# Kernel optimization log

Measured on AMD Instinct MI355X. Metric: run time of the kernel, lower is better.

Reference implementation:

```python
import jax, jax.numpy as jnp
import numpy as np

GRID = (32, 32, 32)  # must match init grid_size


def setup_inputs() -> dict:
    key = jax.random.key(0)
    # Mimic the module's init: D = 0.01 everywhere + 0.1 on the 6x6 diagonal,
    # plus small uniform noise so the baseline exercises non-degenerate values.
    D = jax.random.uniform(key, (6, 6, *GRID), dtype=jnp.float32) * 0.02 + 0.01
    D = D.at[jnp.arange(6), jnp.arange(6)].add(0.1)
    return {"D": D, "sx": 1, "sy": 1, "sz": 1, "ex": 30, "ey": 30, "ez": 30,
            "max_iterations": 300}


def reference(D, sx, sy, sz, ex, ey, ez, max_iterations):
    """flash_wave (training path, inference=False): 300-step CA as one lax.scan.

    Returns the stacked history of phi (pre-update, as the torch loop appends
    phi at the top of each iteration): shape [max_iterations, 6, X, Y, Z].
    Early exit is emulated by freezing phi once the wave reaches (ex,ey,ez),
    so no per-step host sync is needed.
    """
    phi0 = jnp.zeros((6, *GRID), dtype=D.dtype).at[:, sx, sy, sz].set(1.0)
    active_D = D + 0.95  # inference=False branch

    def body(carry, _):
        phi, done = carry
        # 6x6 channel mixing per grid cell: 'oixyz,ixyz->oxyz'
        phi_out = jnp.einsum('oixyz,ixyz->oxyz', active_D, phi)
        pn = jnp.zeros_like(phi)
        pn = pn.at[0, 1:, :, :].set(phi_out[0, :-1, :, :])   # +x
        pn = pn.at[1, :-1, :, :].set(phi_out[1, 1:, :, :])   # -x
        pn = pn.at[2, :, 1:, :].set(phi_out[2, :, :-1, :])   # +y
        pn = pn.at[3, :, :-1, :].set(phi_out[3, :, 1:, :])   # -y
        pn = pn.at[4, :, :, 1:].set(phi_out[4, :, :, :-1])   # +z
        pn = pn.at[5, :, :, :-1].set(phi_out[5, :, :, 1:])   # -z
        nxt = jnp.clip(pn, 0.0, 1.0)
        nxt = jnp.where(done, phi, nxt)  # freeze after target reached
        reached = jnp.sum(nxt[:, ex, ey, ez]) > 0.01
        return (nxt, jnp.logical_or(done, reached)), phi

    (_, _), history = jax.lax.scan(body, (phi0, jnp.array(False)), None,
                                   length=int(max_iterations))
    return history
```

## Files before the change

### kernel.cpp

```cpp
#include <hip/hip_runtime.h>

#define NCH 6
#define NX 32
#define PLANE 1024
#define NCELL (NX * PLANE)
#define STEP_STRIDE (NCH * NCELL)
#define NTHREADS 256
#define NBLOCKS 128
#define RB 2

#define RING32_WORDS ((size_t)RB * 4 * NCELL)
#define F_DONE 0

typedef unsigned long long u64;
typedef unsigned int u32;
typedef float fx4 __attribute__((ext_vector_type(4)));

__device__ __forceinline__ u32 ld32(const u32* p) {
    return __hip_atomic_load(p, __ATOMIC_RELAXED, __HIP_MEMORY_SCOPE_AGENT);
}
__device__ __forceinline__ void st32(u32* p, u32 v) {
    __hip_atomic_store(p, v, __ATOMIC_RELAXED, __HIP_MEMORY_SCOPE_AGENT);
}
__device__ __forceinline__ int ldi(const int* p) {
    return __hip_atomic_load(p, __ATOMIC_RELAXED, __HIP_MEMORY_SCOPE_AGENT);
}
__device__ __forceinline__ void sti(int* p, int v) {
    __hip_atomic_store(p, v, __ATOMIC_RELAXED, __HIP_MEMORY_SCOPE_AGENT);
}
__device__ __forceinline__ u32 tagf(float a, unsigned P) {
    const u32 w = __float_as_uint(a);
    return P ? (w | 0x80000000u) : w;
}
__device__ __forceinline__ float untagf(u32 w) {
    return __uint_as_float(w & 0x7fffffffu);
}

__global__ void __launch_bounds__(NTHREADS)
BEMNA_V7_2_PhaseSpace_44117904064519_kernel(
    const float* __restrict__ D,
    const int* __restrict__ sx_p, const int* __restrict__ sy_p,
    const int* __restrict__ sz_p, const int* __restrict__ ex_p,
    const int* __restrict__ ey_p, const int* __restrict__ ez_p,
    const int* __restrict__ maxit_p,
    float* __restrict__ out,
    u32* __restrict__ ring,
    int* __restrict__ flags)
{
    __shared__ float tile[2][2][NTHREADS];
    __shared__ int lds_dn;

    const int tid = (int)threadIdx.x;
    const int bx  = (int)blockIdx.x;
    const int x   = bx >> 2;
    const int s   = bx & 3;
    const int yl  = tid >> 5;
    const int z   = tid & 31;
    const int y   = (s << 3) + yl;
    const int cell = (x << 10) + (y << 5) + z;

    const int sx = *sx_p, sy = *sy_p, sz = *sz_p;
    const int ex = *ex_p, ey = *ey_p, ez = *ez_p;
    const int maxit = *maxit_p;
    const bool is_seed   = (cell == ((sx << 10) | (sy << 5) | sz));
    const bool is_target = (cell == ((ex << 10) | (ey << 5) | ez));

    float dreg[NCH][NCH];
#pragma unroll
    for (int o = 0; o < NCH; ++o)
#pragma unroll
        for (int i = 0; i < NCH; ++i)
            dreg[o][i] = D[(size_t)(o * NCH + i) * NCELL + cell] + 0.95f;

    const bool has_xm  = (x >= 1), has_xp = (x <= 30);
    const bool edge_ym = (yl == 0), edge_yp = (yl == 7);
    const bool has_ym  = edge_ym && (y >= 1);
    const bool has_yp  = edge_yp && (y <= 30);
    const bool pub_d2  = edge_yp && (y <= 30);
    const bool pub_d3  = edge_ym && (y >= 1);

    const float iv = is_seed ? 1.0f : 0.0f;
    float pz4, pz5;
    {
        float po[NCH];
#pragma unroll
        for (int o = 0; o < NCH; ++o) {
            float a = 0.f;
#pragma unroll
            for (int i = 0; i < NCH; ++i) a = fmaf(dreg[o][i], iv, a);
            po[o] = a;
        }
        st32(ring + 0 * NCELL + cell, tagf(po[0], 0));
        st32(ring + 1 * NCELL + cell, tagf(po[1], 0));
        if (pub_d2) st32(ring + 2 * NCELL + cell, tagf(po[2], 0));
        if (pub_d3) st32(ring + 3 * NCELL + cell, tagf(po[3], 0));
        tile[0][0][tid] = po[2];
        tile[0][1][tid] = po[3];
        pz4 = po[4]; pz5 = po[5];
        float* outp = out + cell;
#pragma unroll
        for (int o = 0; o < NCH; ++o)
            __builtin_nontemporal_store(iv, outp + o * NCELL);
    }
    __syncthreads();

    int tripped = 0;
    for (int t = 0; t <= maxit - 2; ++t) {
        const u32* r = ring + (size_t)(t & 1) * 4 * NCELL;
        const unsigned P = (unsigned)((t >> 1) & 1);

        u32 wxm = 0, wxp = 0, wym = 0, wyp = 0;
        int dn = -1, spins = 0;
        for (;;) {
            if (has_xm) wxm = ld32(r + 0 * NCELL + cell - PLANE);
            if (has_xp) wxp = ld32(r + 1 * NCELL + cell + PLANE);
            if (has_ym) wym = ld32(r + 2 * NCELL + cell - 32);
            if (has_yp) wyp = ld32(r + 3 * NCELL + cell + 32);
            dn = ldi(&flags[F_DONE]);
            bool okr = true;
            if (has_xm) okr = okr & ((wxm >> 31) == P);
            if (has_xp) okr = okr & ((wxp >> 31) == P);
            if (has_ym) okr = okr & ((wym >> 31) == P);
            if (has_yp) okr = okr & ((wyp >> 31) == P);
            if (dn >= 0 && t + 1 > dn) break;
            if (__ballot(okr) == ~0ull) break;
            if (spins++) __builtin_amdgcn_s_sleep(1);
        }
        if (tid == 0) lds_dn = dn;
        __syncthreads();
        if (lds_dn >= 0 && t + 1 > lds_dn) break;

        float v[NCH];
        v[0] = has_xm ? untagf(wxm) : 0.0f;
        v[1] = has_xp ? untagf(wxp) : 0.0f;
        v[2] = edge_ym ? (has_ym ? untagf(wym) : 0.0f) : tile[t & 1][0][tid - 32];
        v[3] = edge_yp ? (has_yp ? untagf(wyp) : 0.0f) : tile[t & 1][1][tid + 32];
        const float s4 = __shfl_up(pz4, 1, 32);
        const float s5 = __shfl_down(pz5, 1, 32);
        v[4] = (z >= 1)  ? s4 : 0.0f;
        v[5] = (z <= 30) ? s5 : 0.0f;
#pragma unroll
        for (int o = 0; o < NCH; ++o) v[o] = fminf(fmaxf(v[o], 0.0f), 1.0f);

        if (is_target && !tripped) {
            if (v[0] + v[1] + v[2] + v[3] + v[4] + v[5] > 0.01f) {
                sti(&flags[F_DONE], t + 1);
                tripped = 1;
            }
        }

        float n0 = 0.f, n1 = 0.f, n2 = 0.f, n3 = 0.f, n4 = 0.f, n5 = 0.f;
#pragma unroll
        for (int i = 0; i < NCH; ++i) {
            n0 = fmaf(dreg[0][i], v[i], n0);
            n1 = fmaf(dreg[1][i], v[i], n1);
            n2 = fmaf(dreg[2][i], v[i], n2);
            n3 = fmaf(dreg[3][i], v[i], n3);
            n4 = fmaf(dreg[4][i], v[i], n4);
            n5 = fmaf(dreg[5][i], v[i], n5);
        }

        {
            const unsigned P1 = (unsigned)(((t + 1) >> 1) & 1);
            u32* w = ring + (size_t)((t + 1) & 1) * 4 * NCELL;
            st32(w + 0 * NCELL + cell, tagf(n0, P1));
            st32(w + 1 * NCELL + cell, tagf(n1, P1));
            if (pub_d2) st32(w + 2 * NCELL + cell, tagf(n2, P1));
            if (pub_d3) st32(w + 3 * NCELL + cell, tagf(n3, P1));
            tile[(t + 1) & 1][0][tid] = n2;
            tile[(t + 1) & 1][1][tid] = n3;
            pz4 = n4; pz5 = n5;
        }

        {
            float* outp = out + (size_t)(t + 1) * STEP_STRIDE + cell;
#pragma unroll
            for (int o = 0; o < NCH; ++o)
                __builtin_nontemporal_store(v[o], outp + o * NCELL);
        }
    }
}

__global__ void fill_kernel(const int* __restrict__ flags,
                            float* __restrict__ outf,
                            int total4)
{
    const int s4 = STEP_STRIDE / 4;
    const int maxit = total4 / s4;
    const int ds = flags[F_DONE];
    const int tf = (ds >= 1 && ds <= maxit - 1) ? ds : maxit - 1;
    const int idx = (int)blockIdx.x * (int)blockDim.x + (int)threadIdx.x;
    fx4* o4 = (fx4*)outf;
    const fx4 v = o4[(size_t)tf * s4 + idx];
    for (int t = tf + 1; t < maxit; ++t)
        __builtin_nontemporal_store(v, &o4[(size_t)t * s4 + idx]);
}

extern "C" void kernel_launch(void* const* d_in, const int* in_sizes, int n_in,
                              void* d_out, int out_size, void* d_ws, size_t ws_size,
                              hipStream_t stream)
{
    const float* D   = (const float*)d_in[0];
    const int* sx    = (const int*)d_in[1];
    const int* sy    = (const int*)d_in[2];
    const int* sz    = (const int*)d_in[3];
    const int* ex    = (const int*)d_in[4];
    const int* ey    = (const int*)d_in[5];
    const int* ez    = (const int*)d_in[6];
    const int* maxit = (const int*)d_in[7];
    float* out = (float*)d_out;

    u32* ring  = (u32*)d_ws;
    int* flags = (int*)(ring + RING32_WORDS);

    BEMNA_V7_2_PhaseSpace_44117904064519_kernel<<<dim3(NBLOCKS), dim3(NTHREADS), 0, stream>>>(
        D, sx, sy, sz, ex, ey, ez, maxit, out, ring, flags);

    const int total4 = out_size / 4;
    fill_kernel<<<dim3((STEP_STRIDE / 4) / 256), dim3(256), 0, stream>>>(
        flags, out, total4);
}
```

Measured before the change: 348.1 us.

## Move y-neighbor exchange to wave shuffles and double-buffer spin polling loads

Half of the in-block y-neighbor values now travel between the two rows held by each 64-lane wave through a cross-half shuffle instead of LDS, so only the other half is still read from the shared tile. The cross-block spin-wait is software-pipelined: the next set of ring and flag loads is issued before the previous set is checked, which hides part of the polling latency. The block barrier is replaced by a hand-written LDS waitcnt plus s_barrier with a scheduling fence. This adds branch divergence between odd and even rows and relies on a subtle pairing of odd/even rows per wave and on the correctness of the custom barrier.

```diff
diff --git a/kernel.cpp b/kernel.cpp
--- a/kernel.cpp
+++ b/kernel.cpp
@@ -34,6 +34,14 @@
 }
 __device__ __forceinline__ float untagf(u32 w) {
     return __uint_as_float(w & 0x7fffffffu);
+}
+__device__ __forceinline__ float clip01(float a) {
+    return fminf(fmaxf(a, 0.0f), 1.0f);
+}
+__device__ __forceinline__ void barrier_lds() {
+    asm volatile("s_waitcnt lgkmcnt(0)" ::: "memory");
+    __builtin_amdgcn_s_barrier();
+    __builtin_amdgcn_sched_barrier(0);
 }
 
 __global__ void __launch_bounds__(NTHREADS)
@@ -78,9 +86,10 @@
     const bool has_yp  = edge_yp && (y <= 30);
     const bool pub_d2  = edge_yp && (y <= 30);
     const bool pub_d3  = edge_ym && (y >= 1);
+    const bool odd     = (yl & 1) != 0;
 
     const float iv = is_seed ? 1.0f : 0.0f;
-    float pz4, pz5;
+    float pn2, pn3, pz4, pz5;
     {
         float po[NCH];
 #pragma unroll
@@ -96,7 +105,7 @@
         if (pub_d3) st32(ring + 3 * NCELL + cell, tagf(po[3], 0));
         tile[0][0][tid] = po[2];
         tile[0][1][tid] = po[3];
-        pz4 = po[4]; pz5 = po[5];
+        pn2 = po[2]; pn3 = po[3]; pz4 = po[4]; pz5 = po[5];
         float* outp = out + cell;
 #pragma unroll
         for (int o = 0; o < NCH; ++o)
@@ -109,55 +118,89 @@
         const u32* r = ring + (size_t)(t & 1) * 4 * NCELL;
         const unsigned P = (unsigned)((t >> 1) & 1);
 
-        u32 wxm = 0, wxp = 0, wym = 0, wyp = 0;
-        int dn = -1, spins = 0;
-        for (;;) {
-            if (has_xm) wxm = ld32(r + 0 * NCELL + cell - PLANE);
-            if (has_xp) wxp = ld32(r + 1 * NCELL + cell + PLANE);
-            if (has_ym) wym = ld32(r + 2 * NCELL + cell - 32);
-            if (has_yp) wyp = ld32(r + 3 * NCELL + cell + 32);
-            dn = ldi(&flags[F_DONE]);
-            bool okr = true;
-            if (has_xm) okr = okr & ((wxm >> 31) == P);
-            if (has_xp) okr = okr & ((wxp >> 31) == P);
-            if (has_ym) okr = okr & ((wym >> 31) == P);
-            if (has_yp) okr = okr & ((wyp >> 31) == P);
-            if (dn >= 0 && t + 1 > dn) break;
-            if (__ballot(okr) == ~0ull) break;
-            if (spins++) __builtin_amdgcn_s_sleep(1);
+        const float rz4 = __shfl_up(pz4, 1, 32);
+        const float rz5 = __shfl_down(pz5, 1, 32);
+        const float v4 = (z >= 1)  ? clip01(rz4) : 0.0f;
+        const float v5 = (z <= 30) ? clip01(rz5) : 0.0f;
+        const float sendw = odd ? pn3 : pn2;
+        const float recvw = __shfl_xor(sendw, 32, 64);
+        float v2 = 0.0f, v3 = 0.0f;
+        if (odd) v2 = clip01(recvw); else v3 = clip01(recvw);
+
+        u32 wxm = 0, wxp = 0, wym = 0, wyp = 0; int dn = -1;
+        {
+            const u32* q0 = r + 0 * NCELL + cell - PLANE;
+            const u32* q1 = r + 1 * NCELL + cell + PLANE;
+            const u32* q2 = r + 2 * NCELL + cell - 32;
+            const u32* q3 = r + 3 * NCELL + cell + 32;
+            u32 axm = 0, axp = 0, aym = 0, ayp = 0;
+            u32 bxm = 0, bxp = 0, bym = 0, byp = 0;
+            int adn, bdn;
+            if (has_xm) axm = ld32(q0);
+            if (has_xp) axp = ld32(q1);
+            if (has_ym) aym = ld32(q2);
+            if (has_yp) ayp = ld32(q3);
+            adn = ldi(&flags[F_DONE]);
+            for (;;) {
+                if (has_xm) bxm = ld32(q0);
+                if (has_xp) bxp = ld32(q1);
+                if (has_ym) bym = ld32(q2);
+                if (has_yp) byp = ld32(q3);
+                bdn = ldi(&flags[F_DONE]);
+                bool okr = true;
+                if (has_xm) okr = okr & ((axm >> 31) == P);
+                if (has_xp) okr = okr & ((axp >> 31) == P);
+                if (has_ym) okr = okr & ((aym >> 31) == P);
+                if (has_yp) okr = okr & ((ayp >> 31) == P);
+                if ((adn >= 0 && t + 1 > adn) || __ballot(okr) == ~0ull) {
+                    wxm = axm; wxp = axp; wym = aym; wyp = ayp; dn = adn; break;
+                }
+                if (has_xm) axm = ld32(q0);
+                if (has_xp) axp = ld32(q1);
+                if (has_ym) aym = ld32(q2);
+                if (has_yp) ayp = ld32(q3);
+                adn = ldi(&flags[F_DONE]);
+                okr = true;
+                if (has_xm) okr = okr & ((bxm >> 31) == P);
+                if (has_xp) okr = okr & ((bxp >> 31) == P);
+                if (has_ym) okr = okr & ((bym >> 31) == P);
+                if (has_yp) okr = okr & ((byp >> 31) == P);
+                if ((bdn >= 0 && t + 1 > bdn) || __ballot(okr) == ~0ull) {
+                    wxm = bxm; wxp = bxp; wym = bym; wyp = byp; dn = bdn; break;
+                }
+            }
         }
         if (tid == 0) lds_dn = dn;
-        __syncthreads();
+        barrier_lds();
         if (lds_dn >= 0 && t + 1 > lds_dn) break;
 
-        float v[NCH];
-        v[0] = has_xm ? untagf(wxm) : 0.0f;
-        v[1] = has_xp ? untagf(wxp) : 0.0f;
-        v[2] = edge_ym ? (has_ym ? untagf(wym) : 0.0f) : tile[t & 1][0][tid - 32];
-        v[3] = edge_yp ? (has_yp ? untagf(wyp) : 0.0f) : tile[t & 1][1][tid + 32];
-        const float s4 = __shfl_up(pz4, 1, 32);
-        const float s5 = __shfl_down(pz5, 1, 32);
-        v[4] = (z >= 1)  ? s4 : 0.0f;
-        v[5] = (z <= 30) ? s5 : 0.0f;
-#pragma unroll
-        for (int o = 0; o < NCH; ++o) v[o] = fminf(fmaxf(v[o], 0.0f), 1.0f);
+        const float v0 = has_xm ? clip01(untagf(wxm)) : 0.0f;
+        const float v1 = has_xp ? clip01(untagf(wxp)) : 0.0f;
+        if (odd) {
+            v3 = (yl <= 5) ? clip01(tile[t & 1][1][tid + 32])
+                           : (has_yp ? clip01(untagf(wyp)) : 0.0f);
+        } else {
+            v2 = (yl >= 2) ? clip01(tile[t & 1][0][tid - 32])
+                           : (has_ym ? clip01(untagf(wym)) : 0.0f);
+        }
 
         if (is_target && !tripped) {
-            if (v[0] + v[1] + v[2] + v[3] + v[4] + v[5] > 0.01f) {
+            if (v0 + v1 + v2 + v3 + v4 + v5 > 0.01f) {
                 sti(&flags[F_DONE], t + 1);
                 tripped = 1;
             }
         }
 
+        const float vv[NCH] = { v0, v1, v2, v3, v4, v5 };
         float n0 = 0.f, n1 = 0.f, n2 = 0.f, n3 = 0.f, n4 = 0.f, n5 = 0.f;
 #pragma unroll
         for (int i = 0; i < NCH; ++i) {
-            n0 = fmaf(dreg[0][i], v[i], n0);
-            n1 = fmaf(dreg[1][i], v[i], n1);
-            n2 = fmaf(dreg[2][i], v[i], n2);
-            n3 = fmaf(dreg[3][i], v[i], n3);
-            n4 = fmaf(dreg[4][i], v[i], n4);
-            n5 = fmaf(dreg[5][i], v[i], n5);
+            n0 = fmaf(dreg[0][i], vv[i], n0);
+            n1 = fmaf(dreg[1][i], vv[i], n1);
+            n2 = fmaf(dreg[2][i], vv[i], n2);
+            n3 = fmaf(dreg[3][i], vv[i], n3);
+            n4 = fmaf(dreg[4][i], vv[i], n4);
+            n5 = fmaf(dreg[5][i], vv[i], n5);
         }
 
         {
@@ -169,14 +212,17 @@
             if (pub_d3) st32(w + 3 * NCELL + cell, tagf(n3, P1));
             tile[(t + 1) & 1][0][tid] = n2;
             tile[(t + 1) & 1][1][tid] = n3;
-            pz4 = n4; pz5 = n5;
+            pn2 = n2; pn3 = n3; pz4 = n4; pz5 = n5;
         }
 
         {
             float* outp = out + (size_t)(t + 1) * STEP_STRIDE + cell;
-#pragma unroll
-            for (int o = 0; o < NCH; ++o)
-                __builtin_nontemporal_store(v[o], outp + o * NCELL);
+            __builtin_nontemporal_store(v0, outp + 0 * NCELL);
+            __builtin_nontemporal_store(v1, outp + 1 * NCELL);
+            __builtin_nontemporal_store(v2, outp + 2 * NCELL);
+            __builtin_nontemporal_store(v3, outp + 3 * NCELL);
+            __builtin_nontemporal_store(v4, outp + 4 * NCELL);
+            __builtin_nontemporal_store(v5, outp + 5 * NCELL);
         }
     }
 }
```

After: 358.1 us. 2.9% more time.
